# Kernel tuning notes

Measured on AMD Instinct MI355X. Metric: run time of the kernel, lower is better.

## Reference

```python
import jax, jax.numpy as jnp
import numpy as np

# static config (matches init_kwargs)
H = 64; W = 64; WS = 8; SHIFT = 4; HEADS = 16; DIM = 512; TED = 512; B = 16
NW = (H // WS) * (W // WS)          # 64 windows
WS2 = WS * WS                        # 64 tokens per window
N = WS2 + 1                          # +1 time-embedding token appended per window
HIDDEN = int(DIM * 4.0)


def _rel_pos_index():
    # standard Swin relative-position index over the WS*WS window tokens
    coords = np.stack(np.meshgrid(np.arange(WS), np.arange(WS), indexing='ij'))  # (2, WS, WS)
    cf = coords.reshape(2, -1)
    rel = (cf[:, :, None] - cf[:, None, :]).transpose(1, 2, 0)  # (WS2, WS2, 2)
    rel[..., 0] += WS - 1
    rel[..., 1] += WS - 1
    rel[..., 0] *= 2 * WS - 1
    return rel.sum(-1)  # (WS2, WS2) int


def _attn_mask():
    # shifted-window attention mask, exactly as built in __init__
    img_mask = np.zeros((H, W), dtype=np.float32)
    slices = (slice(0, -WS), slice(-WS, -SHIFT), slice(-SHIFT, None))
    cnt = 0
    for hs in slices:
        for ws_ in slices:
            img_mask[hs, ws_] = cnt
            cnt += 1
    mw = img_mask.reshape(H // WS, WS, W // WS, WS).transpose(0, 2, 1, 3).reshape(-1, WS2)  # (NW, WS2)
    diff = mw[:, None, :] - mw[:, :, None]
    return np.where(diff != 0, -100.0, 0.0).astype(np.float32)  # (NW, WS2, WS2)


def _ln(x, g, b):
    m = x.mean(-1, keepdims=True)
    v = ((x - m) ** 2).mean(-1, keepdims=True)
    return (x - m) / jnp.sqrt(v + 1e-5) * g + b


def setup_inputs() -> dict:
    key = jax.random.key(0)
    ks = jax.random.split(key, 10)
    s = 0.02
    return {
        'x': jax.random.normal(ks[0], (B, H * W, DIM), dtype=jnp.float32),
        'emb': jax.random.normal(ks[1], (B, TED), dtype=jnp.float32),
        'gamma1': jnp.ones((DIM,), jnp.float32),
        'beta1': jnp.zeros((DIM,), jnp.float32),
        'W_emb': jax.random.normal(ks[2], (TED, DIM), jnp.float32) * s,
        'b_emb': jnp.zeros((DIM,), jnp.float32),
        'W_qkv': jax.random.normal(ks[3], (DIM, 3 * DIM), jnp.float32) * s,
        'b_qkv': jnp.zeros((3 * DIM,), jnp.float32),
        'rel_bias_table': jax.random.normal(ks[4], ((2 * WS - 1) ** 2, HEADS), jnp.float32) * s,
        'W_proj': jax.random.normal(ks[5], (DIM, DIM), jnp.float32) * s,
        'b_proj': jnp.zeros((DIM,), jnp.float32),
        'gamma2': jnp.ones((DIM,), jnp.float32),
        'beta2': jnp.zeros((DIM,), jnp.float32),
        'W1': jax.random.normal(ks[6], (DIM, HIDDEN), jnp.float32) * s,
        'b1': jnp.zeros((HIDDEN,), jnp.float32),
        'W2': jax.random.normal(ks[7], (HIDDEN, DIM), jnp.float32) * s,
        'b2': jnp.zeros((DIM,), jnp.float32),
    }


def reference(x, emb, gamma1, beta1, W_emb, b_emb, W_qkv, b_qkv, rel_bias_table,
              W_proj, b_proj, gamma2, beta2, W1, b1, W2, b2):
    Bb, L, C = x.shape
    hd = C // HEADS
    shortcut = x
    # norm1 -> spatial -> cyclic shift
    xn = _ln(x, gamma1, beta1).reshape(Bb, H, W, C)
    xs = jnp.roll(xn, (-SHIFT, -SHIFT), axis=(1, 2))
    # window partition: (B, NW, WS2, C)
    xw = xs.reshape(Bb, H // WS, WS, W // WS, WS, C).transpose(0, 1, 3, 2, 4, 5)
    xw = xw.reshape(Bb, NW, WS2, C)
    # append time-embedding token to each window
    t = jax.nn.silu(emb) @ W_emb + b_emb                       # (B, C)
    t = jnp.broadcast_to(t[:, None, None, :], (Bb, NW, 1, C))
    xw = jnp.concatenate([xw, t], axis=2).reshape(Bb * NW, N, C)
    # windowed multi-head attention
    qkv = (xw @ W_qkv + b_qkv).reshape(Bb * NW, N, 3, HEADS, hd).transpose(2, 0, 3, 1, 4)
    q, k, v = qkv[0] * (hd ** -0.5), qkv[1], qkv[2]            # (B*NW, HEADS, N, hd)
    attn = jnp.einsum('bhnd,bhmd->bhnm', q, k)
    bias = rel_bias_table[_rel_pos_index().reshape(-1)].reshape(WS2, WS2, HEADS).transpose(2, 0, 1)
    bias = jnp.pad(bias, ((0, 0), (0, 1), (0, 1)))             # zero bias for time token
    attn = attn + bias[None]
    mask = jnp.pad(jnp.asarray(_attn_mask()), ((0, 0), (0, 1), (0, 1)))  # (NW, N, N)
    attn = attn.reshape(Bb, NW, HEADS, N, N) + mask[None, :, None]
    attn = jax.nn.softmax(attn.reshape(Bb * NW, HEADS, N, N), axis=-1)
    out = jnp.einsum('bhnm,bhmd->bnhd', attn, v).reshape(Bb * NW, N, C)
    out = (out @ W_proj + b_proj)[:, :WS2]                     # drop time token
    # window reverse + reverse shift
    out = out.reshape(Bb, H // WS, W // WS, WS, WS, C).transpose(0, 1, 3, 2, 4, 5).reshape(Bb, H, W, C)
    out = jnp.roll(out, (SHIFT, SHIFT), axis=(1, 2)).reshape(Bb, L, C)
    x1 = shortcut + out
    # norm2 + MLP (exact GELU, as torch nn.GELU default)
    hmid = jax.nn.gelu(_ln(x1, gamma2, beta2) @ W1 + b1, approximate=False)
    return x1 + hmid @ W2 + b2
```

## Files before the change

kernel.cpp:

```cpp
#include <hip/hip_runtime.h>
#include <hip/hip_bf16.h>

typedef __hip_bfloat16 bf16;
typedef short short4_t __attribute__((ext_vector_type(4)));
typedef short short8 __attribute__((ext_vector_type(8)));
typedef float f32x4 __attribute__((ext_vector_type(4)));

#define DIMC 512
#define HEADS_ 16
#define NTOK 65
#define NWIN 64
#define NB 16
#define HID 2048
#define TOTROWS 66560
#define ATT_CHUNK_WB 128
#define ATT_CHUNK_ROWS (ATT_CHUNK_WB * NTOK)


__device__ __forceinline__ float b2f(short s) {
  unsigned int u = ((unsigned int)(unsigned short)s) << 16;
  float f; __builtin_memcpy(&f, &u, 4); return f;
}
__device__ __forceinline__ short f2s(float f) {
  bf16 b = __float2bfloat16(f);
  short s; __builtin_memcpy(&s, &b, 2); return s;
}

__device__ __forceinline__ void async_lds16(const bf16* g, bf16* l) {
  __builtin_amdgcn_global_load_lds(
      (const __attribute__((address_space(1))) unsigned int*)g,
      (__attribute__((address_space(3))) unsigned int*)l,
      16, 0, 0);
}

__device__ __forceinline__ void wave_stats512(const float* v, float& m, float& rstd)
{
  float s = 0.0f, ss = 0.0f;
  #pragma unroll
  for (int e = 0; e < 8; ++e) { s += v[e]; ss += v[e] * v[e]; }
  #pragma unroll
  for (int o = 1; o < 64; o <<= 1) { s += __shfl_xor(s, o); ss += __shfl_xor(ss, o); }
  m = s * (1.0f / 512.0f);
  rstd = rsqrtf(ss * (1.0f / 512.0f) - m * m + 1e-5f);
}

__device__ __forceinline__ float gelu_t(float v) {
  float v2 = v * v;
  float a  = fmaf(0.044715f, v2, 1.0f);
  float e  = __builtin_exp2f(-2.3022042f * (v * a));
  return v * __builtin_amdgcn_rcpf(1.0f + e);
}


__global__ __launch_bounds__(256) void time_emb_kernel(
    const float* __restrict__ emb, const float* __restrict__ W_emb,
    const float* __restrict__ b_emb, float* __restrict__ t)
{
  int b = blockIdx.x;
  int c = blockIdx.y * 256 + threadIdx.x;
  __shared__ float se[512];
  for (int k = threadIdx.x; k < 512; k += 256) {
    float e = emb[b * 512 + k];
    se[k] = e / (1.0f + expf(-e));
  }
  __syncthreads();
  float acc = b_emb[c];
  for (int k = 0; k < 512; ++k) acc += se[k] * W_emb[k * 512 + c];
  t[b * 512 + c] = acc;
}

__global__ void transpose_cast_kernel(const float* __restrict__ W, bf16* __restrict__ Wt,
                                      int Kd, int Nd)
{
  __shared__ float tile[32][33];
  int n0 = blockIdx.x * 32, k0 = blockIdx.y * 32;
  for (int r = threadIdx.y; r < 32; r += 8)
    tile[r][threadIdx.x] = W[(long)(k0 + r) * Nd + n0 + threadIdx.x];
  __syncthreads();
  for (int r = threadIdx.y; r < 32; r += 8)
    Wt[(long)(n0 + r) * Kd + k0 + threadIdx.x] = __float2bfloat16(tile[threadIdx.x][r]);
}

__global__ __launch_bounds__(256) void bias_mask_kernel(
    const float* __restrict__ btab, float* __restrict__ tbl)
{
  int h = blockIdx.x, wt = blockIdx.y;
  for (int idx = threadIdx.x; idx < 6400; idx += 256) {
    int i = idx / 80, t = idx % 80;
    float v;
    if (t >= 65) v = -1e30f;
    else if (i >= 64 || t == 64) v = 0.0f;
    else {
      int rel = (((i >> 3) - (t >> 3) + 7) * 15) + ((i & 7) - (t & 7) + 7);
      v = btab[rel * HEADS_ + h];
      int rci = (wt & 2) ? (((i >> 3) < 4) ? 1 : 2) : 0;
      int cci = (wt & 1) ? (((i & 7) < 4) ? 1 : 2) : 0;
      int rct = (wt & 2) ? (((t >> 3) < 4) ? 1 : 2) : 0;
      int cct = (wt & 1) ? (((t & 7) < 4) ? 1 : 2) : 0;
      if (rci * 3 + cci != rct * 3 + cct) v -= 100.0f;
    }
    tbl[(h * 4 + wt) * 6400 + idx] = v;
  }
}

__global__ __launch_bounds__(256) void ln1_window_kernel(
    const float* __restrict__ x, const float* __restrict__ gamma,
    const float* __restrict__ beta, const float* __restrict__ t,
    bf16* __restrict__ xw)
{
  long r = (long)blockIdx.x * 4 + (threadIdx.x >> 6);
  int lane = threadIdx.x & 63;
  int wb = (int)(r / NTOK), i = (int)(r % NTOK);
  int b = wb >> 6, w = wb & 63;
  bf16* out = xw + r * 512 + lane * 8;
  if (i == 64) {
    const float* tr = t + b * 512 + lane * 8;
    short8 o;
    #pragma unroll
    for (int e = 0; e < 8; ++e) o[e] = f2s(tr[e]);
    *(short8*)out = o;
    return;
  }
  int wh = w >> 3, ww = w & 7, ih = i >> 3, iw = i & 7;
  int hsrc = ((wh * 8 + ih) + 4) & 63;
  int wsrc = ((ww * 8 + iw) + 4) & 63;
  const float* xr = x + ((long)b * 4096 + hsrc * 64 + wsrc) * 512 + lane * 8;
  float v[8];
  *(f32x4*)&v[0] = *(const f32x4*)xr;
  *(f32x4*)&v[4] = *(const f32x4*)(xr + 4);
  float m, rstd;
  wave_stats512(v, m, rstd);
  const float* g = gamma + lane * 8;
  const float* bt = beta + lane * 8;
  short8 o;
  #pragma unroll
  for (int e = 0; e < 8; ++e) o[e] = f2s((v[e] - m) * rstd * g[e] + bt[e]);
  *(short8*)out = o;
}

__global__ __launch_bounds__(256) void ln2_kernel(
    const float* __restrict__ x1, const float* __restrict__ gamma,
    const float* __restrict__ beta, bf16* __restrict__ out)
{
  long r = (long)blockIdx.x * 4 + (threadIdx.x >> 6);
  int lane = threadIdx.x & 63;
  const float* xr = x1 + r * 512 + lane * 8;
  float v[8];
  *(f32x4*)&v[0] = *(const f32x4*)xr;
  *(f32x4*)&v[4] = *(const f32x4*)(xr + 4);
  float m, rstd;
  wave_stats512(v, m, rstd);
  const float* g = gamma + lane * 8;
  const float* bt = beta + lane * 8;
  short8 o;
  #pragma unroll
  for (int e = 0; e < 8; ++e) o[e] = f2s((v[e] - m) * rstd * g[e] + bt[e]);
  *(short8*)(out + r * 512 + lane * 8) = o;
}

template<int EPI, int K>
__global__ __launch_bounds__(256, 3) void gemmk_kernel(
    const bf16* __restrict__ A, const bf16* __restrict__ Bt,
    const float* __restrict__ bias, int N, int nx,
    bf16* __restrict__ outB, float* __restrict__ outF,
    const float* __restrict__ xin, int rowOffset)
{
  constexpr int NKT = K / 32;
  static_assert((NKT - 1) % 3 == 0, "triplet peel needs NKT = 3m+1");
  __shared__ bf16 lA[3][128 * 32];
  __shared__ bf16 lB[3][128 * 32];
  const int tid = threadIdx.x;
  const int lane = tid & 63, wv = tid >> 6;
  const int wm = wv >> 1, wn = wv & 1;
  const int fr = lane & 15, fg = lane >> 4;

  const int nwg = gridDim.x, bid = blockIdx.x;
  const int q8 = nwg >> 3, rr8 = nwg & 7;
  const int xcd = bid & 7, idx = bid >> 3;
  const int sid = (xcd < rr8 ? xcd * (q8 + 1) : rr8 * (q8 + 1) + (xcd - rr8) * q8) + idx;
  const long row0 = (long)(sid / nx) * 128;
  const long col0 = (long)(sid % nx) * 128;

  const int rl = lane >> 2, sp = lane & 3;
  const int s = sp ^ ((rl >> 1) & 3);
  const bf16* ga0 = A  + (row0 + wv * 32 + rl) * (long)K + s * 8;
  const bf16* ga1 = ga0 + 16 * (long)K;
  const bf16* gb0 = Bt + (col0 + wv * 32 + rl) * (long)K + s * 8;
  const bf16* gb1 = gb0 + 16 * (long)K;

  f32x4 acc[4][4] = {};
  const int swr = (fg ^ ((fr >> 1) & 3)) << 4;

  auto stage = [&](int buf, int t) {
    const long o = (long)t * 32;
    async_lds16(ga0 + o, &lA[buf][(wv * 32) * 32]);
    async_lds16(ga1 + o, &lA[buf][(wv * 32 + 16) * 32]);
    async_lds16(gb0 + o, &lB[buf][(wv * 32) * 32]);
    async_lds16(gb1 + o, &lB[buf][(wv * 32 + 16) * 32]);
  };

  stage(0, 0);
  stage(1, 1);

#define GBODY(BUF)                                                              \
  do {                                                                          \
    if (t + 1 < NKT) asm volatile("s_waitcnt vmcnt(4)" ::: "memory");           \
    else             asm volatile("s_waitcnt vmcnt(0)" ::: "memory");           \
    __builtin_amdgcn_s_barrier();                                               \
    short8 bfv[4], af[4];                                                       \
    _Pragma("unroll")                                                           \
    for (int ni = 0; ni < 4; ++ni)                                              \
      bfv[ni] = *(const short8*)((const char*)&lB[BUF][0] +                     \
                                 (wn * 64 + ni * 16 + fr) * 64 + swr);          \
    _Pragma("unroll")                                                           \
    for (int mi = 0; mi < 4; ++mi)                                              \
      af[mi] = *(const short8*)((const char*)&lA[BUF][0] +                      \
                                (wm * 64 + mi * 16 + fr) * 64 + swr);           \
    if (t + 2 < NKT) stage((BUF + 2) % 3, t + 2);                               \
    __builtin_amdgcn_s_setprio(1);                                              \
    _Pragma("unroll")                                                           \
    for (int mi = 0; mi < 4; ++mi)                                              \
      _Pragma("unroll")                                                         \
      for (int ni = 0; ni < 4; ++ni)                                            \
        acc[mi][ni] = __builtin_amdgcn_mfma_f32_16x16x32_bf16(                  \
            af[mi], bfv[ni], acc[mi][ni], 0, 0, 0);                             \
    __builtin_amdgcn_s_setprio(0);                                              \
    ++t;                                                                        \
  } while (0)

  int t = 0;
  GBODY(0);
  for (int g = 0; g < (NKT - 1) / 3; ++g) {
    GBODY(1);
    GBODY(2);
    GBODY(0);
  }
#undef GBODY

  if (EPI == 2 || EPI == 3) {
    __syncthreads();
    float* ep = (float*)&lA[0][0];
    const int l31 = lane & 31, lr2 = lane >> 5;
    const f32x4 b4 = *(const f32x4*)&bias[col0 + l31 * 4];
    #pragma unroll
    for (int h = 0; h < 2; ++h) {
      if (wm == h) {
        #pragma unroll
        for (int mi = 0; mi < 4; ++mi)
          #pragma unroll
          for (int ni = 0; ni < 4; ++ni)
            #pragma unroll
            for (int j = 0; j < 4; ++j)
              ep[(mi * 16 + fg * 4 + j) * 132 + wn * 64 + ni * 16 + fr] = acc[mi][ni][j];
      }
      __syncthreads();
      #pragma unroll
      for (int it = 0; it < 8; ++it) {
        int lrow = it * 8 + wv * 2 + lr2;
        long rr = row0 + h * 64 + lrow;
        f32x4 v = *(const f32x4*)&ep[lrow * 132 + l31 * 4];
        v += b4;
        if (EPI == 2) {
          int grow = rowOffset + (int)rr;
          int ii = grow % NTOK;
          if (ii != 64) {
            int wb = grow / NTOK;
            int b = wb >> 6, w = wb & 63;
            int wh = w >> 3, ww = w & 7, ih = ii >> 3, iw = ii & 7;
            int hh   = ((wh * 8 + ih) + 4) & 63;
            int wcol = ((ww * 8 + iw) + 4) & 63;
            long o = ((long)b * 4096 + hh * 64 + wcol) * 512 + col0 + l31 * 4;
            f32x4 xi = *(const f32x4*)&xin[o];
            *(f32x4*)&outF[o] = xi + v;
          }
        } else {
          long o = rr * N + col0 + l31 * 4;
          f32x4 ov = *(const f32x4*)&outF[o];
          *(f32x4*)&outF[o] = ov + v;
        }
      }
      __syncthreads();
    }
    return;
  }

  float bs[4];
  #pragma unroll
  for (int ni = 0; ni < 4; ++ni) bs[ni] = bias[col0 + wn * 64 + ni * 16 + fr];
  #pragma unroll
  for (int mi = 0; mi < 4; ++mi) {
    #pragma unroll
    for (int j = 0; j < 4; ++j) {
      long rr = row0 + wm * 64 + mi * 16 + fg * 4 + j;
      #pragma unroll
      for (int ni = 0; ni < 4; ++ni) {
        long cc = col0 + wn * 64 + ni * 16 + fr;
        float v = acc[mi][ni][j] + bs[ni];
        if (EPI == 0) {
          outB[rr * N + cc] = __float2bfloat16(v);
        } else {
          outB[rr * N + cc] = __float2bfloat16(gelu_t(v));
        }
      }
    }
  }
}

__global__ __launch_bounds__(64, 2) void attn_mfma_kernel(
    const bf16* __restrict__ qkv, bf16* __restrict__ attnO,
    const float* __restrict__ tbl, int wb0)
{
  __shared__ bf16 P[80 * 104];
  const int lwb = blockIdx.x, h = blockIdx.y;
  const int lane = threadIdx.x;
  const int fr = lane & 15, g = lane >> 4;
  const float scale = 0.17677669529663687f;
  const bf16* base = qkv + (long)lwb * 65 * 1536 + h * 32 + g * 8;

  for (int idx = lane; idx < 240; idx += 64) {
    int i = idx / 3, sl = idx % 3;
    *(short8*)&P[i * 104 + 80 + sl * 8] = (short8){0, 0, 0, 0, 0, 0, 0, 0};
  }

  short8 bq[5];
  #pragma unroll
  for (int tn = 0; tn < 5; ++tn) {
    int qr = tn * 16 + fr; qr = qr > 64 ? 64 : qr;
    bq[tn] = *(const short8*)(base + (long)qr * 1536);
  }

  f32x4 acc[5][5];
  #pragma unroll
  for (int tm = 0; tm < 5; ++tm) {
    int kr = tm * 16 + fr; kr = kr > 64 ? 64 : kr;
    short8 ak = *(const short8*)(base + 512 + (long)kr * 1536);
    #pragma unroll
    for (int tn = 0; tn < 5; ++tn)
      acc[tm][tn] = __builtin_amdgcn_mfma_f32_16x16x32_bf16(
          ak, bq[tn], (f32x4){0.0f, 0.0f, 0.0f, 0.0f}, 0, 0, 0);
  }

  const int w = (wb0 + lwb) & 63;
  const int wt = (((w >> 3) == 7) ? 2 : 0) + (((w & 7) == 7) ? 1 : 0);
  const float* tp = tbl + (h * 4 + wt) * 6400;
  #pragma unroll
  for (int tn = 0; tn < 5; ++tn) {
    const int i = tn * 16 + fr;
    const float* ti = tp + i * 80 + g * 4;
    float m = -3.0e38f;
    #pragma unroll
    for (int tm = 0; tm < 5; ++tm) {
      f32x4 bv = *(const f32x4*)(ti + tm * 16);
      #pragma unroll
      for (int r = 0; r < 4; ++r) {
        float sv = fmaf(acc[tm][tn][r], scale, bv[r]);
        acc[tm][tn][r] = sv;
        m = fmaxf(m, sv);
      }
    }
    m = fmaxf(m, __shfl_xor(m, 16));
    m = fmaxf(m, __shfl_xor(m, 32));
    float l = 0.0f;
    #pragma unroll
    for (int tm = 0; tm < 5; ++tm)
      #pragma unroll
      for (int r = 0; r < 4; ++r) {
        float e = __expf(acc[tm][tn][r] - m);
        acc[tm][tn][r] = e;
        l += e;
      }
    l += __shfl_xor(l, 16);
    l += __shfl_xor(l, 32);
    float inv = 1.0f / l;
    #pragma unroll
    for (int tm = 0; tm < 5; ++tm) {
      short4_t pk;
      #pragma unroll
      for (int r = 0; r < 4; ++r) pk[r] = f2s(acc[tm][tn][r] * inv);
      *(short4_t*)&P[i * 104 + tm * 16 + g * 4] = pk;
    }
  }

  const bf16* vbase = qkv + (long)lwb * 65 * 1536 + 1024 + h * 32;
  f32x4 oacc[2][5] = {};
  #pragma unroll
  for (int kt = 0; kt < 3; ++kt) {
    short8 bp[5];
    #pragma unroll
    for (int tn = 0; tn < 5; ++tn)
      bp[tn] = *(const short8*)&P[(tn * 16 + fr) * 104 + kt * 32 + g * 8];
    #pragma unroll
    for (int ma = 0; ma < 2; ++ma) {
      short8 av;
      #pragma unroll
      for (int e = 0; e < 8; ++e) {
        int vr = kt * 32 + g * 8 + e; vr = vr > 64 ? 64 : vr;
        av[e] = *(const short*)(vbase + (long)vr * 1536 + ma * 16 + fr);
      }
      #pragma unroll
      for (int tn = 0; tn < 5; ++tn)
        oacc[ma][tn] = __builtin_amdgcn_mfma_f32_16x16x32_bf16(
            av, bp[tn], oacc[ma][tn], 0, 0, 0);
    }
  }

  #pragma unroll
  for (int tn = 0; tn < 5; ++tn) {
    int i = tn * 16 + fr;
    if (i < 65) {
      bf16* op = attnO + (long)(lwb * 65 + i) * 512 + h * 32 + g * 4;
      #pragma unroll
      for (int ma = 0; ma < 2; ++ma) {
        short4_t o4;
        #pragma unroll
        for (int r = 0; r < 4; ++r) o4[r] = f2s(oacc[ma][tn][r]);
        *(short4_t*)(op + ma * 16) = o4;
      }
    }
  }
}


extern "C" void kernel_launch(void* const* d_in, const int* in_sizes, int n_in,
                              void* d_out, int out_size, void* d_ws, size_t ws_size,
                              hipStream_t stream)
{
  const float* x      = (const float*)d_in[0];
  const float* emb    = (const float*)d_in[1];
  const float* gamma1 = (const float*)d_in[2];
  const float* beta1  = (const float*)d_in[3];
  const float* W_emb  = (const float*)d_in[4];
  const float* b_emb  = (const float*)d_in[5];
  const float* W_qkv  = (const float*)d_in[6];
  const float* b_qkv  = (const float*)d_in[7];
  const float* btab   = (const float*)d_in[8];
  const float* W_proj = (const float*)d_in[9];
  const float* b_proj = (const float*)d_in[10];
  const float* gamma2 = (const float*)d_in[11];
  const float* beta2  = (const float*)d_in[12];
  const float* W1     = (const float*)d_in[13];
  const float* b1     = (const float*)d_in[14];
  const float* W2     = (const float*)d_in[15];
  const float* b2     = (const float*)d_in[16];
  float* out = (float*)d_out;
  (void)n_in; (void)in_sizes; (void)out_size;

  char* ws = (char*)d_ws;
  size_t off = 0;
  auto alloc = [&](size_t bytes) -> char* {
    char* p = ws + off;
    off += (bytes + 255) & ~(size_t)255;
    return p;
  };
  bf16* wt_qkv  = (bf16*)alloc((size_t)1536 * 512 * 2);
  bf16* wt_proj = (bf16*)alloc((size_t)512 * 512 * 2);
  bf16* wt1     = (bf16*)alloc((size_t)2048 * 512 * 2);
  bf16* wt2     = (bf16*)alloc((size_t)512 * 2048 * 2);
  float* tvec   = (float*)alloc((size_t)16 * 512 * 4);
  float* tbl    = (float*)alloc((size_t)16 * 4 * 6400 * 4);

  const size_t sz_xw    = (size_t)TOTROWS * 512 * 2;
  const size_t sz_qkv   = (size_t)TOTROWS * 1536 * 2;
  const size_t sz_attnO = (size_t)TOTROWS * 512 * 2;
  const bool big = ws_size >= off + sz_xw + sz_qkv + sz_attnO + (4u << 20);

  transpose_cast_kernel<<<dim3(1536 / 32, 512 / 32), dim3(32, 8), 0, stream>>>(W_qkv, wt_qkv, 512, 1536);
  transpose_cast_kernel<<<dim3(512 / 32, 512 / 32),  dim3(32, 8), 0, stream>>>(W_proj, wt_proj, 512, 512);
  transpose_cast_kernel<<<dim3(2048 / 32, 512 / 32), dim3(32, 8), 0, stream>>>(W1, wt1, 512, 2048);
  transpose_cast_kernel<<<dim3(512 / 32, 2048 / 32), dim3(32, 8), 0, stream>>>(W2, wt2, 2048, 512);
  time_emb_kernel<<<dim3(16, 2), 256, 0, stream>>>(emb, W_emb, b_emb, tvec);
  bias_mask_kernel<<<dim3(16, 4), 256, 0, stream>>>(btab, tbl);

  if (big) {
    bf16* xw    = (bf16*)alloc(sz_xw);
    bf16* qkv   = (bf16*)alloc(sz_qkv);
    bf16* attnO = (bf16*)alloc(sz_attnO);
    bf16* ln2b  = xw;
    bf16* h     = qkv;

    ln1_window_kernel<<<TOTROWS / 4, 256, 0, stream>>>(x, gamma1, beta1, tvec, xw);
    gemmk_kernel<0, 512><<<12 * 520, 256, 0, stream>>>(
        xw, wt_qkv, b_qkv, 1536, 12, qkv, nullptr, nullptr, 0);
    attn_mfma_kernel<<<dim3(NB * NWIN, HEADS_), 64, 0, stream>>>(qkv, attnO, tbl, 0);
    gemmk_kernel<2, 512><<<4 * 520, 256, 0, stream>>>(
        attnO, wt_proj, b_proj, 512, 4, nullptr, out, x, 0);
    ln2_kernel<<<65536 / 4, 256, 0, stream>>>(out, gamma2, beta2, ln2b);
    gemmk_kernel<1, 512><<<16 * 512, 256, 0, stream>>>(
        ln2b, wt1, b1, 2048, 16, h, nullptr, nullptr, 0);
    gemmk_kernel<3, 2048><<<4 * 512, 256, 0, stream>>>(
        h, wt2, b2, 512, 4, nullptr, out, nullptr, 0);
  } else {
    char* regionA = alloc(sz_xw);
    bf16* xw   = (bf16*)regionA;
    bf16* ln2b = (bf16*)regionA;
    bf16* qkv_c = (bf16*)alloc((size_t)ATT_CHUNK_ROWS * 1536 * 2);
    char* regionB = alloc(sz_attnO);
    bf16* attnO = (bf16*)regionB;
    bf16* h_c   = (bf16*)regionB;

    ln1_window_kernel<<<TOTROWS / 4, 256, 0, stream>>>(x, gamma1, beta1, tvec, xw);
    for (int ac = 0; ac < 8; ++ac) {
      long r0 = (long)ac * ATT_CHUNK_ROWS;
      gemmk_kernel<0, 512><<<12 * 65, 256, 0, stream>>>(
          xw + r0 * 512, wt_qkv, b_qkv, 1536, 12, qkv_c, nullptr, nullptr, 0);
      attn_mfma_kernel<<<dim3(ATT_CHUNK_WB, HEADS_), 64, 0, stream>>>(
          qkv_c, attnO + r0 * 512, tbl, ac * ATT_CHUNK_WB);
    }
    gemmk_kernel<2, 512><<<4 * 520, 256, 0, stream>>>(
        attnO, wt_proj, b_proj, 512, 4, nullptr, out, x, 0);
    ln2_kernel<<<65536 / 4, 256, 0, stream>>>(out, gamma2, beta2, ln2b);
    for (int mc = 0; mc < 4; ++mc) {
      long r0 = (long)mc * 16384;
      gemmk_kernel<1, 512><<<16 * 128, 256, 0, stream>>>(
          ln2b + r0 * 512, wt1, b1, 2048, 16, h_c, nullptr, nullptr, 0);
      gemmk_kernel<3, 2048><<<4 * 128, 256, 0, stream>>>(
          h_c, wt2, b2, 512, 4, nullptr, out + r0 * 512, nullptr, 0);
    }
  }
}
```

Before: 904.2 us.

## Store residual x1 in bf16 and chunk MLP to keep hidden activations cache-resident

```diff
diff --git a/kernel.cpp b/kernel.cpp
--- a/kernel.cpp
+++ b/kernel.cpp
@@ -13,6 +13,7 @@
 #define NB 16
 #define HID 2048
 #define TOTROWS 66560
+#define IMGROWS 65536
 #define ATT_CHUNK_WB 128
 #define ATT_CHUNK_ROWS (ATT_CHUNK_WB * NTOK)
 
@@ -139,15 +140,15 @@
 }
 
 __global__ __launch_bounds__(256) void ln2_kernel(
-    const float* __restrict__ x1, const float* __restrict__ gamma,
+    const bf16* __restrict__ x1, const float* __restrict__ gamma,
     const float* __restrict__ beta, bf16* __restrict__ out)
 {
   long r = (long)blockIdx.x * 4 + (threadIdx.x >> 6);
   int lane = threadIdx.x & 63;
-  const float* xr = x1 + r * 512 + lane * 8;
+  short8 xv = *(const short8*)(x1 + r * 512 + lane * 8);
   float v[8];
-  *(f32x4*)&v[0] = *(const f32x4*)xr;
-  *(f32x4*)&v[4] = *(const f32x4*)(xr + 4);
+  #pragma unroll
+  for (int e = 0; e < 8; ++e) v[e] = b2f(xv[e]);
   float m, rstd;
   wave_stats512(v, m, rstd);
   const float* g = gamma + lane * 8;
@@ -163,12 +164,13 @@
     const bf16* __restrict__ A, const bf16* __restrict__ Bt,
     const float* __restrict__ bias, int N, int nx,
     bf16* __restrict__ outB, float* __restrict__ outF,
-    const float* __restrict__ xin, int rowOffset)
+    const float* __restrict__ xinF, const bf16* __restrict__ xinB, int rowOffset)
 {
   constexpr int NKT = K / 32;
   static_assert((NKT - 1) % 3 == 0, "triplet peel needs NKT = 3m+1");
-  __shared__ bf16 lA[3][128 * 32];
-  __shared__ bf16 lB[3][128 * 32];
+  __shared__ bf16 ldsbuf[6 * 128 * 32];
+  bf16* const lAp = ldsbuf;
+  bf16* const lBp = ldsbuf + 3 * 4096;
   const int tid = threadIdx.x;
   const int lane = tid & 63, wv = tid >> 6;
   const int wm = wv >> 1, wn = wv & 1;
@@ -193,10 +195,10 @@
 
   auto stage = [&](int buf, int t) {
     const long o = (long)t * 32;
-    async_lds16(ga0 + o, &lA[buf][(wv * 32) * 32]);
-    async_lds16(ga1 + o, &lA[buf][(wv * 32 + 16) * 32]);
-    async_lds16(gb0 + o, &lB[buf][(wv * 32) * 32]);
-    async_lds16(gb1 + o, &lB[buf][(wv * 32 + 16) * 32]);
+    async_lds16(ga0 + o, &lAp[buf * 4096 + (wv * 32) * 32]);
+    async_lds16(ga1 + o, &lAp[buf * 4096 + (wv * 32 + 16) * 32]);
+    async_lds16(gb0 + o, &lBp[buf * 4096 + (wv * 32) * 32]);
+    async_lds16(gb1 + o, &lBp[buf * 4096 + (wv * 32 + 16) * 32]);
   };
 
   stage(0, 0);
@@ -210,13 +212,13 @@
     short8 bfv[4], af[4];                                                       \
     _Pragma("unroll")                                                           \
     for (int ni = 0; ni < 4; ++ni)                                              \
-      bfv[ni] = *(const short8*)((const char*)&lB[BUF][0] +                     \
+      bfv[ni] = *(const short8*)((const char*)&lBp[(BUF) * 4096] +              \
                                  (wn * 64 + ni * 16 + fr) * 64 + swr);          \
     _Pragma("unroll")                                                           \
     for (int mi = 0; mi < 4; ++mi)                                              \
-      af[mi] = *(const short8*)((const char*)&lA[BUF][0] +                      \
+      af[mi] = *(const short8*)((const char*)&lAp[(BUF) * 4096] +               \
                                 (wm * 64 + mi * 16 + fr) * 64 + swr);           \
-    if (t + 2 < NKT) stage((BUF + 2) % 3, t + 2);                               \
+    if (t + 2 < NKT) stage(((BUF) + 2) % 3, t + 2);                             \
     __builtin_amdgcn_s_setprio(1);                                              \
     _Pragma("unroll")                                                           \
     for (int mi = 0; mi < 4; ++mi)                                              \
@@ -239,7 +241,7 @@
 
   if (EPI == 2 || EPI == 3) {
     __syncthreads();
-    float* ep = (float*)&lA[0][0];
+    float* ep = (float*)ldsbuf;
     const int l31 = lane & 31, lr2 = lane >> 5;
     const f32x4 b4 = *(const f32x4*)&bias[col0 + l31 * 4];
     #pragma unroll
@@ -270,13 +272,20 @@
             int hh   = ((wh * 8 + ih) + 4) & 63;
             int wcol = ((ww * 8 + iw) + 4) & 63;
             long o = ((long)b * 4096 + hh * 64 + wcol) * 512 + col0 + l31 * 4;
-            f32x4 xi = *(const f32x4*)&xin[o];
-            *(f32x4*)&outF[o] = xi + v;
+            f32x4 xi = *(const f32x4*)&xinF[o];
+            f32x4 x1 = xi + v;
+            short4_t s4;
+            #pragma unroll
+            for (int e = 0; e < 4; ++e) s4[e] = f2s(x1[e]);
+            *(short4_t*)&outB[o] = s4;
           }
         } else {
           long o = rr * N + col0 + l31 * 4;
-          f32x4 ov = *(const f32x4*)&outF[o];
-          *(f32x4*)&outF[o] = ov + v;
+          short4_t xv = *(const short4_t*)&xinB[o];
+          f32x4 xf;
+          #pragma unroll
+          for (int e = 0; e < 4; ++e) xf[e] = b2f(xv[e]);
+          *(f32x4*)&outF[o] = xf + v;
         }
       }
       __syncthreads();
@@ -472,49 +481,56 @@
   bias_mask_kernel<<<dim3(16, 4), 256, 0, stream>>>(btab, tbl);
 
   if (big) {
-    bf16* xw    = (bf16*)alloc(sz_xw);
-    bf16* qkv   = (bf16*)alloc(sz_qkv);
-    bf16* attnO = (bf16*)alloc(sz_attnO);
-    bf16* ln2b  = xw;
-    bf16* h     = qkv;
+    char* regionA = alloc(sz_xw);
+    char* regionQ = alloc(sz_qkv);
+    bf16* attnO   = (bf16*)alloc(sz_attnO);
+    bf16* xw   = (bf16*)regionA;
+    bf16* x1b  = (bf16*)regionA;
+    bf16* qkv  = (bf16*)regionQ;
+    bf16* h_c  = (bf16*)regionQ;
+    bf16* ln2b = (bf16*)(regionQ + (size_t)32768 * 2048 * 2);
 
     ln1_window_kernel<<<TOTROWS / 4, 256, 0, stream>>>(x, gamma1, beta1, tvec, xw);
     gemmk_kernel<0, 512><<<12 * 520, 256, 0, stream>>>(
-        xw, wt_qkv, b_qkv, 1536, 12, qkv, nullptr, nullptr, 0);
+        xw, wt_qkv, b_qkv, 1536, 12, qkv, nullptr, nullptr, nullptr, 0);
     attn_mfma_kernel<<<dim3(NB * NWIN, HEADS_), 64, 0, stream>>>(qkv, attnO, tbl, 0);
     gemmk_kernel<2, 512><<<4 * 520, 256, 0, stream>>>(
-        attnO, wt_proj, b_proj, 512, 4, nullptr, out, x, 0);
-    ln2_kernel<<<65536 / 4, 256, 0, stream>>>(out, gamma2, beta2, ln2b);
-    gemmk_kernel<1, 512><<<16 * 512, 256, 0, stream>>>(
-        ln2b, wt1, b1, 2048, 16, h, nullptr, nullptr, 0);
-    gemmk_kernel<3, 2048><<<4 * 512, 256, 0, stream>>>(
-        h, wt2, b2, 512, 4, nullptr, out, nullptr, 0);
+        attnO, wt_proj, b_proj, 512, 4, x1b, nullptr, x, nullptr, 0);
+    ln2_kernel<<<IMGROWS / 4, 256, 0, stream>>>(x1b, gamma2, beta2, ln2b);
+    for (int mc = 0; mc < 2; ++mc) {
+      long r0 = (long)mc * 32768;
+      gemmk_kernel<1, 512><<<16 * 256, 256, 0, stream>>>(
+          ln2b + r0 * 512, wt1, b1, 2048, 16, h_c, nullptr, nullptr, nullptr, 0);
+      gemmk_kernel<3, 2048><<<4 * 256, 256, 0, stream>>>(
+          h_c, wt2, b2, 512, 4, nullptr, out + r0 * 512, nullptr, x1b + r0 * 512, 0);
+    }
   } else {
     char* regionA = alloc(sz_xw);
     bf16* xw   = (bf16*)regionA;
-    bf16* ln2b = (bf16*)regionA;
+    bf16* x1b  = (bf16*)regionA;
     bf16* qkv_c = (bf16*)alloc((size_t)ATT_CHUNK_ROWS * 1536 * 2);
     char* regionB = alloc(sz_attnO);
     bf16* attnO = (bf16*)regionB;
-    bf16* h_c   = (bf16*)regionB;
+    bf16* ln2b  = (bf16*)regionB;
+    bf16* h_c   = (bf16*)alloc((size_t)16384 * 2048 * 2);
 
     ln1_window_kernel<<<TOTROWS / 4, 256, 0, stream>>>(x, gamma1, beta1, tvec, xw);
     for (int ac = 0; ac < 8; ++ac) {
       long r0 = (long)ac * ATT_CHUNK_ROWS;
       gemmk_kernel<0, 512><<<12 * 65, 256, 0, stream>>>(
-          xw + r0 * 512, wt_qkv, b_qkv, 1536, 12, qkv_c, nullptr, nullptr, 0);
+          xw + r0 * 512, wt_qkv, b_qkv, 1536, 12, qkv_c, nullptr, nullptr, nullptr, 0);
       attn_mfma_kernel<<<dim3(ATT_CHUNK_WB, HEADS_), 64, 0, stream>>>(
           qkv_c, attnO + r0 * 512, tbl, ac * ATT_CHUNK_WB);
     }
     gemmk_kernel<2, 512><<<4 * 520, 256, 0, stream>>>(
-        attnO, wt_proj, b_proj, 512, 4, nullptr, out, x, 0);
-    ln2_kernel<<<65536 / 4, 256, 0, stream>>>(out, gamma2, beta2, ln2b);
+        attnO, wt_proj, b_proj, 512, 4, x1b, nullptr, x, nullptr, 0);
+    ln2_kernel<<<IMGROWS / 4, 256, 0, stream>>>(x1b, gamma2, beta2, ln2b);
     for (int mc = 0; mc < 4; ++mc) {
       long r0 = (long)mc * 16384;
       gemmk_kernel<1, 512><<<16 * 128, 256, 0, stream>>>(
-          ln2b + r0 * 512, wt1, b1, 2048, 16, h_c, nullptr, nullptr, 0);
+          ln2b + r0 * 512, wt1, b1, 2048, 16, h_c, nullptr, nullptr, nullptr, 0);
       gemmk_kernel<3, 2048><<<4 * 128, 256, 0, stream>>>(
-          h_c, wt2, b2, 512, 4, nullptr, out + r0 * 512, nullptr, 0);
-    }
-  }
-}
+          h_c, wt2, b2, 512, 4, nullptr, out + r0 * 512, nullptr, x1b + r0 * 512, 0);
+    }
+  }
+}
```

New measurement: 822.2 us, median of 2. -9.1%, faster.
